# Performance work log

Measured on AMD Instinct MI355X. Metric: run time of the kernel, lower is better.

## Reference

```python
import jax, jax.numpy as jnp
import numpy as np

B, H, W = 4, 64, 64
DIM, HEADS, HEAD = 768, 12, 64
WIN = 14
MLP_DIM = 4 * DIM
EPS = 1e-5


def _ln(x, g, b):
    mu = jnp.mean(x, axis=-1, keepdims=True)
    var = jnp.mean(jnp.square(x - mu), axis=-1, keepdims=True)
    return (x - mu) * jax.lax.rsqrt(var + EPS) * g + b


def _window_partition(x):
    Bb, Hh, Ww, C = x.shape
    pad_h = (WIN - Hh % WIN) % WIN
    pad_w = (WIN - Ww % WIN) % WIN
    x = jnp.pad(x, ((0, 0), (0, pad_h), (0, pad_w), (0, 0)))
    Hp, Wp = Hh + pad_h, Ww + pad_w
    x = x.reshape(Bb, Hp // WIN, WIN, Wp // WIN, WIN, C)
    win = x.transpose(0, 1, 3, 2, 4, 5).reshape(-1, WIN, WIN, C)
    return win, (Hp, Wp)


def _window_unpartition(win, pad_hw, hw):
    Hp, Wp = pad_hw
    Hh, Ww = hw
    Bb = win.shape[0] // (Hp * Wp // WIN // WIN)
    x = win.reshape(Bb, Hp // WIN, Wp // WIN, WIN, WIN, -1)
    x = x.transpose(0, 1, 3, 2, 4, 5).reshape(Bb, Hp, Wp, -1)
    return x[:, :Hh, :Ww, :]


def _attention(xw, qkv_w, qkv_b, proj_w, proj_b, rel_pos_h, rel_pos_w):
    Bw = xw.shape[0]
    N = WIN * WIN
    qkv = xw.reshape(Bw, N, DIM) @ qkv_w + qkv_b            # [Bw, N, 3*DIM]
    qkv = qkv.reshape(Bw, N, 3, HEADS, HEAD)
    qkv = qkv.transpose(2, 0, 3, 1, 4).reshape(3, Bw * HEADS, N, HEAD)
    q, k, v = qkv[0], qkv[1], qkv[2]
    scale = HEAD ** -0.5
    attn = jnp.einsum('bqc,bkc->bqk', q * scale, k)         # [Bw*HEADS, N, N]
    # decomposed relative position bias (q_size == k_size => plain gather)
    idx = jnp.arange(WIN)[:, None] - jnp.arange(WIN)[None, :] + (WIN - 1)
    Rh = rel_pos_h[idx]
    Rw = rel_pos_w[idx]
    r_q = q.reshape(-1, WIN, WIN, HEAD)
    rel_h = jnp.einsum('bhwc,hkc->bhwk', r_q, Rh)
    rel_w = jnp.einsum('bhwc,wkc->bhwk', r_q, Rw)
    attn = attn.reshape(-1, WIN, WIN, WIN, WIN) + rel_h[..., None] + rel_w[..., None, :]
    attn = jax.nn.softmax(attn.reshape(-1, N, N), axis=-1)
    out = attn @ v                                          # [Bw*HEADS, N, HEAD]
    out = out.reshape(Bw, HEADS, WIN, WIN, HEAD).transpose(0, 2, 3, 1, 4)
    out = out.reshape(Bw, WIN, WIN, DIM)
    return out @ proj_w + proj_b


def setup_inputs() -> dict:
    key = jax.random.key(0)
    ks = jax.random.split(key, 8)
    s = 0.02
    return {
        'x': jax.random.normal(ks[0], (B, H, W, DIM), jnp.float32),
        'norm1_g': jnp.ones((DIM,), jnp.float32),
        'norm1_b': jnp.zeros((DIM,), jnp.float32),
        'qkv_w': jax.random.normal(ks[1], (DIM, 3 * DIM), jnp.float32) * s,
        'qkv_b': jnp.zeros((3 * DIM,), jnp.float32),
        'proj_w': jax.random.normal(ks[2], (DIM, DIM), jnp.float32) * s,
        'proj_b': jnp.zeros((DIM,), jnp.float32),
        'rel_pos_h': jax.random.normal(ks[3], (2 * WIN - 1, HEAD), jnp.float32) * s,
        'rel_pos_w': jax.random.normal(ks[4], (2 * WIN - 1, HEAD), jnp.float32) * s,
        'norm2_g': jnp.ones((DIM,), jnp.float32),
        'norm2_b': jnp.zeros((DIM,), jnp.float32),
        'mlp_w1': jax.random.normal(ks[5], (DIM, MLP_DIM), jnp.float32) * s,
        'mlp_b1': jnp.zeros((MLP_DIM,), jnp.float32),
        'mlp_w2': jax.random.normal(ks[6], (MLP_DIM, DIM), jnp.float32) * s,
        'mlp_b2': jnp.zeros((DIM,), jnp.float32),
    }


def reference(x, norm1_g, norm1_b, qkv_w, qkv_b, proj_w, proj_b,
              rel_pos_h, rel_pos_w, norm2_g, norm2_b,
              mlp_w1, mlp_b1, mlp_w2, mlp_b2):
    shortcut = x
    x = _ln(x, norm1_g, norm1_b)
    win, pad_hw = _window_partition(x)
    win = _attention(win, qkv_w, qkv_b, proj_w, proj_b, rel_pos_h, rel_pos_w)
    x = _window_unpartition(win, pad_hw, (H, W))
    x = shortcut + x
    y = _ln(x, norm2_g, norm2_b)
    y = jax.nn.gelu(y @ mlp_w1 + mlp_b1, approximate=False) @ mlp_w2 + mlp_b2
    return x + y
```

## Files before the change

kernel.cpp:

```cpp
#include <hip/hip_runtime.h>
#include <hip/hip_bf16.h>
#include <math.h>

#define DIMC 768
#define NHEADS 12
#define WINSZ 14
#define NTOK 196
#define TOKENS 16384

using bf = __hip_bfloat16;
typedef __attribute__((ext_vector_type(4))) float f32x4;
typedef __attribute__((ext_vector_type(8))) short bf16x8;

typedef __attribute__((address_space(3))) void lds_void_t;
typedef const __attribute__((address_space(1))) void gmem_void_t;

__device__ inline float bfu2f(ushort u) { return __uint_as_float((uint)u << 16); }
__device__ inline ushort f2bu(float f) {
    bf t = __float2bfloat16(f);
    return __builtin_bit_cast(ushort, t);
}

__global__ __launch_bounds__(256) void transpose_k(const float* __restrict__ in,
                                                   ushort* __restrict__ out, int R, int C) {
    long i = (long)blockIdx.x * 256 + threadIdx.x;
    if (i >= (long)R * C) return;
    int r = (int)(i / C), c = (int)(i % C);
    out[(long)c * R + r] = f2bu(in[i]);
}

__device__ inline float blk_sum(float v, float* wred, int tid) {
    for (int m = 32; m; m >>= 1) v += __shfl_xor(v, m);
    if ((tid & 63) == 0) wred[tid >> 6] = v;
    __syncthreads();
    float r = wred[0] + wred[1] + wred[2] + wred[3];
    __syncthreads();
    return r;
}

__global__ __launch_bounds__(256) void ln_k(const float* __restrict__ x, const float* __restrict__ g,
                                            const float* __restrict__ bb, ushort* __restrict__ out) {
    int row = blockIdx.x, tid = threadIdx.x;
    const float* xr = x + (size_t)row * DIMC;
    __shared__ float wred[4];
    float v0 = xr[tid], v1 = xr[tid + 256], v2 = xr[tid + 512];
    float mean = blk_sum(v0 + v1 + v2, wred, tid) * (1.f / 768.f);
    float d0 = v0 - mean, d1 = v1 - mean, d2 = v2 - mean;
    float var = blk_sum(d0 * d0 + d1 * d1 + d2 * d2, wred, tid) * (1.f / 768.f);
    float rs = rsqrtf(var + 1e-5f);
    ushort* o = out + (size_t)row * DIMC;
    o[tid]       = f2bu(d0 * rs * g[tid]       + bb[tid]);
    o[tid + 256] = f2bu(d1 * rs * g[tid + 256] + bb[tid + 256]);
    o[tid + 512] = f2bu(d2 * rs * g[tid + 512] + bb[tid + 512]);
}

enum { EPI_BIAS = 0, EPI_GELU = 1, EPI_PROJRES = 2, EPI_ACC = 3, EPI_RESOUT = 4 };

template <int EPI>
__global__ __launch_bounds__(256) void gemm_k(const ushort* __restrict__ A, int lda,
                                              const ushort* __restrict__ Bt, int ldb,
                                              const float* __restrict__ bias,
                                              ushort* __restrict__ outb,
                                              float* __restrict__ outf,
                                              const float* __restrict__ xorig,
                                              float* __restrict__ x2,
                                              int N, int K) {
    __shared__ ushort lA0[2][128 * 32];
    __shared__ ushort lA1[2][128 * 32];
    __shared__ ushort lB0[2][128 * 32];
    __shared__ ushort lB1[2][128 * 32];

    const int nwg = gridDim.x * gridDim.y;
    const int l = blockIdx.y * gridDim.x + blockIdx.x;
    const int nl = (l & 7) * (nwg >> 3) + (l >> 3);
    const int bx = nl % gridDim.x, by = nl / gridDim.x;
    const int bm = by * 128, bn = bx * 128;

    const int tid = threadIdx.x, wave = tid >> 6, lane = tid & 63;
    const int wy = wave >> 1, wx = wave & 1;
    const int lm = lane & 15, quad = lane >> 4;

    f32x4 acc[4][4];
#pragma unroll
    for (int r = 0; r < 4; ++r)
#pragma unroll
        for (int s = 0; s < 4; ++s) acc[r][s] = (f32x4){0.f, 0.f, 0.f, 0.f};

    const int c0 = wave * 2, c1 = wave * 2 + 1;
    const int srcg = (lane & 3) ^ ((lane >> 3) & 3);
    const ushort* Ab = A + (size_t)(bm + (lane >> 2)) * lda + srcg * 8;
    const ushort* Bb = Bt + (size_t)(bn + (lane >> 2)) * ldb + srcg * 8;
    const size_t a16 = (size_t)16 * lda, b16 = (size_t)16 * ldb;

    auto stage = [&](int bi, int k0) {
        __builtin_amdgcn_global_load_lds((gmem_void_t*)(Ab + (size_t)c0 * a16 + k0),
                                         (lds_void_t*)&lA0[bi][c0 * 512], 16, 0, 0);
        __builtin_amdgcn_global_load_lds((gmem_void_t*)(Ab + (size_t)c0 * a16 + k0 + 32),
                                         (lds_void_t*)&lA1[bi][c0 * 512], 16, 0, 0);
        __builtin_amdgcn_global_load_lds((gmem_void_t*)(Ab + (size_t)c1 * a16 + k0),
                                         (lds_void_t*)&lA0[bi][c1 * 512], 16, 0, 0);
        __builtin_amdgcn_global_load_lds((gmem_void_t*)(Ab + (size_t)c1 * a16 + k0 + 32),
                                         (lds_void_t*)&lA1[bi][c1 * 512], 16, 0, 0);
        __builtin_amdgcn_global_load_lds((gmem_void_t*)(Bb + (size_t)c0 * b16 + k0),
                                         (lds_void_t*)&lB0[bi][c0 * 512], 16, 0, 0);
        __builtin_amdgcn_global_load_lds((gmem_void_t*)(Bb + (size_t)c0 * b16 + k0 + 32),
                                         (lds_void_t*)&lB1[bi][c0 * 512], 16, 0, 0);
        __builtin_amdgcn_global_load_lds((gmem_void_t*)(Bb + (size_t)c1 * b16 + k0),
                                         (lds_void_t*)&lB0[bi][c1 * 512], 16, 0, 0);
        __builtin_amdgcn_global_load_lds((gmem_void_t*)(Bb + (size_t)c1 * b16 + k0 + 32),
                                         (lds_void_t*)&lB1[bi][c1 * 512], 16, 0, 0);
    };

    const int rg = (quad ^ ((lm >> 1) & 3)) * 8;
    const int nt = K >> 6;

    stage(0, 0);
    __syncthreads();

    for (int t = 0; t < nt; ++t) {
        const int cur = t & 1;
        if (t + 1 < nt) stage(cur ^ 1, (t + 1) * 64);

        bf16x8 af0[4], af1[4], bv0[4], bv1[4];
#pragma unroll
        for (int r = 0; r < 4; ++r) {
            af0[r] = *(const bf16x8*)&lA0[cur][(wy * 64 + r * 16 + lm) * 32 + rg];
            af1[r] = *(const bf16x8*)&lA1[cur][(wy * 64 + r * 16 + lm) * 32 + rg];
        }
#pragma unroll
        for (int s = 0; s < 4; ++s) {
            bv0[s] = *(const bf16x8*)&lB0[cur][(wx * 64 + s * 16 + lm) * 32 + rg];
            bv1[s] = *(const bf16x8*)&lB1[cur][(wx * 64 + s * 16 + lm) * 32 + rg];
        }
#pragma unroll
        for (int r = 0; r < 4; ++r)
#pragma unroll
            for (int s = 0; s < 4; ++s) {
                acc[r][s] = __builtin_amdgcn_mfma_f32_16x16x32_bf16(af0[r], bv0[s], acc[r][s], 0, 0, 0);
                acc[r][s] = __builtin_amdgcn_mfma_f32_16x16x32_bf16(af1[r], bv1[s], acc[r][s], 0, 0, 0);
            }
        __syncthreads();
    }

#pragma unroll
    for (int s = 0; s < 4; ++s) {
        int col = bn + wx * 64 + s * 16 + lm;
        float bvl = (EPI == EPI_ACC) ? 0.f : bias[col];
#pragma unroll
        for (int r = 0; r < 4; ++r) {
#pragma unroll
            for (int i = 0; i < 4; ++i) {
                int row = bm + wy * 64 + r * 16 + quad * 4 + i;
                float v = acc[r][s][i] + bvl;
                size_t idx = (size_t)row * N + col;
                if constexpr (EPI == EPI_BIAS) {
                    outb[idx] = f2bu(v);
                } else if constexpr (EPI == EPI_GELU) {
                    outb[idx] = f2bu(0.5f * v * (1.f + erff(v * 0.70710678118f)));
                } else if constexpr (EPI == EPI_PROJRES) {
                    x2[idx] = xorig[idx] + v;
                } else if constexpr (EPI == EPI_ACC) {
                    x2[idx] += v;
                } else {
                    outf[idx] = x2[idx] + v;
                }
            }
        }
    }
}

__global__ __launch_bounds__(256) void attn_k(const ushort* __restrict__ qkv,
                                              const float* __restrict__ qkvb,
                                              const float* __restrict__ relh,
                                              const float* __restrict__ relw,
                                              ushort* __restrict__ aout) {
    const int win = blockIdx.x / NHEADS, head = blockIdx.x % NHEADS;
    const int b = win / 25, wi = win % 25, wr = wi / 5, wc = wi % 5;
    const int hmax = (wr == 4) ? 8 : WINSZ, wmax = (wc == 4) ? 8 : WINSZ;
    const int hoff = head * 64;
    const int tid = threadIdx.x, wave = tid >> 6, lane = tid & 63;
    const int c = lane & 15, quad = lane >> 4;

    __shared__ ushort Ksw[224 * 64];
    __shared__ ushort vTs[64 * 264];
    __shared__ ushort wscr[4][640];

    for (int t = tid; t < 224 * 8; t += 256) {
        int n = t >> 3, ck = t & 7;
        int kh = n >> 4, kw = n & 15;
        uint4 vals;
        if (kw < WINSZ && kh < hmax && kw < wmax) {
            size_t tok = ((size_t)(b * 64 + wr * WINSZ + kh) * 64 + wc * WINSZ + kw);
            vals = *(const uint4*)(qkv + tok * 2304 + 768 + hoff + ck * 8);
        } else if (kw < WINSZ) {
            union { uint4 u; ushort s[8]; } tmp;
#pragma unroll
            for (int j = 0; j < 8; ++j) tmp.s[j] = f2bu(qkvb[768 + hoff + ck * 8 + j]);
            vals = tmp.u;
        } else {
            vals = (uint4){0u, 0u, 0u, 0u};
        }
        *(uint4*)&Ksw[n * 64 + ((ck ^ (n & 7)) * 8)] = vals;
    }
    for (int t = tid; t < 224 * 8; t += 256) {
        int n = t >> 3, dg = t & 7;
        int kh = n >> 4, kw = n & 15;
        union { uint4 u; ushort s[8]; } vals;
        if (kw < WINSZ && kh < hmax && kw < wmax) {
            size_t tok = ((size_t)(b * 64 + wr * WINSZ + kh) * 64 + wc * WINSZ + kw);
            vals.u = *(const uint4*)(qkv + tok * 2304 + 1536 + hoff + dg * 8);
        } else if (kw < WINSZ) {
#pragma unroll
            for (int j = 0; j < 8; ++j) vals.s[j] = f2bu(qkvb[1536 + hoff + dg * 8 + j]);
        } else {
            vals.u = (uint4){0u, 0u, 0u, 0u};
        }
        int kchunk = n >> 3;
#pragma unroll
        for (int j = 0; j < 8; ++j) {
            int d = dg * 8 + j;
            vTs[d * 264 + ((kchunk ^ dg) * 8) + (n & 7)] = vals.s[j];
        }
    }
    __syncthreads();

    bf16x8 rhB[2][2], rwB[2][2];
#pragma unroll
    for (int nt = 0; nt < 2; ++nt) {
        int j = nt * 16 + c; if (j > 26) j = 26;
#pragma unroll
        for (int ks = 0; ks < 2; ++ks) {
            const float* ph = relh + (size_t)j * 64 + ks * 32 + quad * 8;
            const float* pw = relw + (size_t)j * 64 + ks * 32 + quad * 8;
            bf16x8 h, w;
#pragma unroll
            for (int e = 0; e < 8; ++e) {
                h[e] = (short)f2bu(ph[e]);
                w[e] = (short)f2bu(pw[e]);
            }
            rhB[nt][ks] = h; rwB[nt][ks] = w;
        }
    }

    ushort* scr = &wscr[wave][0];
    const int lane48 = lane & 48;

    for (int qh = wave; qh < hmax; qh += 4) {
        int qw = c < wmax ? c : (wmax - 1);
        size_t qtok = ((size_t)(b * 64 + wr * WINSZ + qh) * 64 + wc * WINSZ + qw);
        bf16x8 aq0 = *(const bf16x8*)(qkv + qtok * 2304 + hoff + quad * 8);
        bf16x8 aq1 = *(const bf16x8*)(qkv + qtok * 2304 + hoff + 32 + quad * 8);

        f32x4 z = (f32x4){0.f, 0.f, 0.f, 0.f};
        f32x4 dh0 = __builtin_amdgcn_mfma_f32_16x16x32_bf16(aq0, rhB[0][0], z, 0, 0, 0);
        dh0 = __builtin_amdgcn_mfma_f32_16x16x32_bf16(aq1, rhB[0][1], dh0, 0, 0, 0);
        f32x4 dh1 = __builtin_amdgcn_mfma_f32_16x16x32_bf16(aq0, rhB[1][0], z, 0, 0, 0);
        dh1 = __builtin_amdgcn_mfma_f32_16x16x32_bf16(aq1, rhB[1][1], dh1, 0, 0, 0);
        f32x4 dw0 = __builtin_amdgcn_mfma_f32_16x16x32_bf16(aq0, rwB[0][0], z, 0, 0, 0);
        dw0 = __builtin_amdgcn_mfma_f32_16x16x32_bf16(aq1, rwB[0][1], dw0, 0, 0, 0);
        f32x4 dw1 = __builtin_amdgcn_mfma_f32_16x16x32_bf16(aq0, rwB[1][0], z, 0, 0, 0);
        dw1 = __builtin_amdgcn_mfma_f32_16x16x32_bf16(aq1, rwB[1][1], dw1, 0, 0, 0);

#pragma unroll
        for (int i = 0; i < 4; ++i) {
            scr[(quad * 4 + i) * 28 + c] = f2bu(dh0[i]);
            if (c < 12) scr[(quad * 4 + i) * 28 + 16 + c] = f2bu(dh1[i]);
        }

        float bw[4];
#pragma unroll
        for (int i = 0; i < 4; ++i) {
            int m = quad * 4 + i;
            int j = m - c + 13; int jc = j < 0 ? 0 : j;
            int addr = (lane48 | (jc & 15)) << 2;
            int t0 = __builtin_amdgcn_ds_bpermute(addr, __float_as_int(dw0[i]));
            int t1 = __builtin_amdgcn_ds_bpermute(addr, __float_as_int(dw1[i]));
            bw[i] = (jc >= 16) ? __int_as_float(t1) : __int_as_float(t0);
        }

        f32x4 s[14];
#pragma unroll
        for (int kh = 0; kh < 14; ++kh) {
            int n = kh * 16 + c;
            int n7 = n & 7;
            bf16x8 kb0 = *(const bf16x8*)&Ksw[n * 64 + ((0 * 4 + quad) ^ n7) * 8];
            bf16x8 kb1 = *(const bf16x8*)&Ksw[n * 64 + ((1 * 4 + quad) ^ n7) * 8];
            f32x4 acc = __builtin_amdgcn_mfma_f32_16x16x32_bf16(aq0, kb0, z, 0, 0, 0);
            acc = __builtin_amdgcn_mfma_f32_16x16x32_bf16(aq1, kb1, acc, 0, 0, 0);
            int jstar = qh + 13 - kh;
#pragma unroll
            for (int i = 0; i < 4; ++i) {
                float dh = bfu2f(scr[(quad * 4 + i) * 28 + jstar]);
                float v = fmaf(0.125f, acc[i], dh + bw[i]);
                acc[i] = (c < WINSZ) ? v : -1e30f;
            }
            s[kh] = acc;
        }

        float inv[4];
#pragma unroll
        for (int i = 0; i < 4; ++i) {
            float mx = s[0][i];
#pragma unroll
            for (int kh = 1; kh < 14; ++kh) mx = fmaxf(mx, s[kh][i]);
            mx = fmaxf(mx, __shfl_xor(mx, 1));
            mx = fmaxf(mx, __shfl_xor(mx, 2));
            mx = fmaxf(mx, __shfl_xor(mx, 4));
            mx = fmaxf(mx, __shfl_xor(mx, 8));
            float sum = 0.f;
#pragma unroll
            for (int kh = 0; kh < 14; ++kh) {
                float e = __expf(s[kh][i] - mx);
                s[kh][i] = e;
                sum += e;
            }
            sum += __shfl_xor(sum, 1);
            sum += __shfl_xor(sum, 2);
            sum += __shfl_xor(sum, 4);
            sum += __shfl_xor(sum, 8);
            inv[i] = 1.f / sum;
        }

        f32x4 o[4] = {z, z, z, z};
#pragma unroll
        for (int cc = 0; cc < 7; ++cc) {
#pragma unroll
            for (int i = 0; i < 4; ++i) {
                scr[(quad * 4 + i) * 40 + c]      = f2bu(s[2 * cc][i] * inv[i]);
                scr[(quad * 4 + i) * 40 + 16 + c] = f2bu(s[2 * cc + 1][i] * inv[i]);
            }
            bf16x8 ap = *(const bf16x8*)&scr[c * 40 + quad * 8];
#pragma unroll
            for (int vt = 0; vt < 4; ++vt) {
                int d = vt * 16 + c;
                int dgr = (d >> 3) & 7;
                bf16x8 vb = *(const bf16x8*)&vTs[d * 264 + (((cc * 4 + quad) ^ dgr) * 8)];
                o[vt] = __builtin_amdgcn_mfma_f32_16x16x32_bf16(ap, vb, o[vt], 0, 0, 0);
            }
        }

#pragma unroll
        for (int i = 0; i < 4; ++i) {
            int qwp = quad * 4 + i;
            if (qwp < wmax) {
                size_t otok = ((size_t)(b * 64 + wr * WINSZ + qh) * 64 + wc * WINSZ + qwp);
#pragma unroll
                for (int vt = 0; vt < 4; ++vt)
                    aout[otok * 768 + hoff + vt * 16 + c] = f2bu(o[vt][i]);
            }
        }
    }
}

extern "C" void kernel_launch(void* const* d_in, const int* in_sizes, int n_in,
                              void* d_out, int out_size, void* d_ws, size_t ws_size,
                              hipStream_t stream) {
    const float* x      = (const float*)d_in[0];
    const float* n1g    = (const float*)d_in[1];
    const float* n1b    = (const float*)d_in[2];
    const float* qkv_w  = (const float*)d_in[3];
    const float* qkv_b  = (const float*)d_in[4];
    const float* proj_w = (const float*)d_in[5];
    const float* proj_b = (const float*)d_in[6];
    const float* relh   = (const float*)d_in[7];
    const float* relw   = (const float*)d_in[8];
    const float* n2g    = (const float*)d_in[9];
    const float* n2b    = (const float*)d_in[10];
    const float* w1     = (const float*)d_in[11];
    const float* b1     = (const float*)d_in[12];
    const float* w2     = (const float*)d_in[13];
    const float* b2     = (const float*)d_in[14];
    float* out = (float*)d_out;

    char* ws = (char*)d_ws;
    size_t off = 0;
    auto alloc = [&](size_t bytes) -> void* {
        void* p = ws + off;
        off += (bytes + 255) & ~(size_t)255;
        return p;
    };

    ushort* lnbuf  = (ushort*)alloc((size_t)TOKENS * DIMC * 2);
    ushort* qkvbuf = (ushort*)alloc((size_t)TOKENS * 2304 * 2);
    float* x2      = (float*)alloc((size_t)TOKENS * DIMC * 4);
    ushort* qkvT   = (ushort*)alloc((size_t)2304 * 768 * 2);
    ushort* projT  = (ushort*)alloc((size_t)768 * 768 * 2);
    ushort* w1T    = (ushort*)alloc((size_t)3072 * 768 * 2);
    ushort* w2T    = (ushort*)alloc((size_t)768 * 3072 * 2);
    ushort* aout   = lnbuf;
    ushort* hc     = qkvbuf;

    transpose_k<<<(768 * 2304 + 255) / 256, 256, 0, stream>>>(qkv_w, qkvT, 768, 2304);
    transpose_k<<<(768 * 768 + 255) / 256, 256, 0, stream>>>(proj_w, projT, 768, 768);
    transpose_k<<<(768 * 3072 + 255) / 256, 256, 0, stream>>>(w1, w1T, 768, 3072);
    transpose_k<<<(3072 * 768 + 255) / 256, 256, 0, stream>>>(w2, w2T, 3072, 768);

    ln_k<<<TOKENS, 256, 0, stream>>>(x, n1g, n1b, lnbuf);

    dim3 gq(2304 / 128, TOKENS / 128);
    gemm_k<EPI_BIAS><<<gq, 256, 0, stream>>>(lnbuf, DIMC, qkvT, DIMC, qkv_b, qkvbuf,
                                             nullptr, nullptr, nullptr, 2304, DIMC);

    attn_k<<<100 * NHEADS, 256, 0, stream>>>(qkvbuf, qkv_b, relh, relw, aout);

    dim3 gp(DIMC / 128, TOKENS / 128);
    gemm_k<EPI_PROJRES><<<gp, 256, 0, stream>>>(aout, DIMC, projT, DIMC, proj_b, nullptr,
                                                nullptr, x, x2, DIMC, DIMC);

    ln_k<<<TOKENS, 256, 0, stream>>>(x2, n2g, n2b, lnbuf);

    dim3 gh(1536 / 128, TOKENS / 128);
    for (int c = 0; c < 2; ++c) {
        gemm_k<EPI_GELU><<<gh, 256, 0, stream>>>(lnbuf, DIMC, w1T + (size_t)c * 1536 * 768, DIMC,
                                                 b1 + c * 1536, hc, nullptr, nullptr, nullptr,
                                                 1536, DIMC);
        if (c == 0)
            gemm_k<EPI_ACC><<<gp, 256, 0, stream>>>(hc, 1536, w2T + (size_t)c * 1536, 3072,
                                                    b2, nullptr, nullptr, nullptr, x2, DIMC, 1536);
        else
            gemm_k<EPI_RESOUT><<<gp, 256, 0, stream>>>(hc, 1536, w2T + (size_t)c * 1536, 3072,
                                                       b2, nullptr, out, nullptr, x2, DIMC, 1536);
    }
}
```

Measured before the change: 678.7 us.

## Read K fragments directly from global memory instead of staging in LDS

Removes the shared-memory K tile and its cooperative fill loop. Each wave now loads its K MFMA operands straight from the qkv buffer per key row, substituting the broadcast key bias for padded positions. Occupancy is also hinted with launch_bounds(256,4), since LDS use drops by about 28KB. The trade is repeated global/L2 reads of K by every wave and per-query-row iteration instead of one shared staging pass, which adds latency inside the inner MFMA loop.

```diff
diff --git a/kernel.cpp b/kernel.cpp
--- a/kernel.cpp
+++ b/kernel.cpp
@@ -169,11 +169,11 @@
     }
 }
 
-__global__ __launch_bounds__(256) void attn_k(const ushort* __restrict__ qkv,
-                                              const float* __restrict__ qkvb,
-                                              const float* __restrict__ relh,
-                                              const float* __restrict__ relw,
-                                              ushort* __restrict__ aout) {
+__global__ __launch_bounds__(256, 4) void attn_k(const ushort* __restrict__ qkv,
+                                                 const float* __restrict__ qkvb,
+                                                 const float* __restrict__ relh,
+                                                 const float* __restrict__ relw,
+                                                 ushort* __restrict__ aout) {
     const int win = blockIdx.x / NHEADS, head = blockIdx.x % NHEADS;
     const int b = win / 25, wi = win % 25, wr = wi / 5, wc = wi % 5;
     const int hmax = (wr == 4) ? 8 : WINSZ, wmax = (wc == 4) ? 8 : WINSZ;
@@ -181,27 +181,9 @@
     const int tid = threadIdx.x, wave = tid >> 6, lane = tid & 63;
     const int c = lane & 15, quad = lane >> 4;
 
-    __shared__ ushort Ksw[224 * 64];
     __shared__ ushort vTs[64 * 264];
     __shared__ ushort wscr[4][640];
 
-    for (int t = tid; t < 224 * 8; t += 256) {
-        int n = t >> 3, ck = t & 7;
-        int kh = n >> 4, kw = n & 15;
-        uint4 vals;
-        if (kw < WINSZ && kh < hmax && kw < wmax) {
-            size_t tok = ((size_t)(b * 64 + wr * WINSZ + kh) * 64 + wc * WINSZ + kw);
-            vals = *(const uint4*)(qkv + tok * 2304 + 768 + hoff + ck * 8);
-        } else if (kw < WINSZ) {
-            union { uint4 u; ushort s[8]; } tmp;
-#pragma unroll
-            for (int j = 0; j < 8; ++j) tmp.s[j] = f2bu(qkvb[768 + hoff + ck * 8 + j]);
-            vals = tmp.u;
-        } else {
-            vals = (uint4){0u, 0u, 0u, 0u};
-        }
-        *(uint4*)&Ksw[n * 64 + ((ck ^ (n & 7)) * 8)] = vals;
-    }
     for (int t = tid; t < 224 * 8; t += 256) {
         int n = t >> 3, dg = t & 7;
         int kh = n >> 4, kw = n & 15;
@@ -241,6 +223,18 @@
             rhB[nt][ks] = h; rwB[nt][ks] = w;
         }
     }
+
+    bf16x8 kbias0, kbias1;
+#pragma unroll
+    for (int j = 0; j < 8; ++j) {
+        kbias0[j] = (short)f2bu(qkvb[768 + hoff + quad * 8 + j]);
+        kbias1[j] = (short)f2bu(qkvb[768 + hoff + 32 + quad * 8 + j]);
+    }
+    const int ccl = (c < wmax) ? c : (wmax - 1);
+    const bool cval = (c < wmax);
+    const ushort* Kp = qkv + ((size_t)(b * 64 + wr * WINSZ) * 64 + wc * WINSZ + ccl) * 2304
+                     + 768 + hoff + quad * 8;
+    const size_t krow = (size_t)64 * 2304;
 
     ushort* scr = &wscr[wave][0];
     const int lane48 = lane & 48;
@@ -281,10 +275,16 @@
         f32x4 s[14];
 #pragma unroll
         for (int kh = 0; kh < 14; ++kh) {
-            int n = kh * 16 + c;
-            int n7 = n & 7;
-            bf16x8 kb0 = *(const bf16x8*)&Ksw[n * 64 + ((0 * 4 + quad) ^ n7) * 8];
-            bf16x8 kb1 = *(const bf16x8*)&Ksw[n * 64 + ((1 * 4 + quad) ^ n7) * 8];
+            bf16x8 kb0, kb1;
+            if (kh < 8 || kh < hmax) {
+                const ushort* p = Kp + (size_t)kh * krow;
+                bf16x8 g0 = *(const bf16x8*)p;
+                bf16x8 g1 = *(const bf16x8*)(p + 32);
+                kb0 = cval ? g0 : kbias0;
+                kb1 = cval ? g1 : kbias1;
+            } else {
+                kb0 = kbias0; kb1 = kbias1;
+            }
             f32x4 acc = __builtin_amdgcn_mfma_f32_16x16x32_bf16(aq0, kb0, z, 0, 0, 0);
             acc = __builtin_amdgcn_mfma_f32_16x16x32_bf16(aq1, kb1, acc, 0, 0, 0);
             int jstar = qh + 13 - kh;
```

Result: slower. 885.7 us (+30.5%).

## Process two query rows per wave in attention to reuse K/V LDS fragments

Applied to the files above, without the earlier changes.

The attention kernel now has each wave handle two query rows at once (qh and qh+4), sharing each loaded K and V fragment across two MFMA chains. Per-wave scratch is doubled to hold bias and probability tiles for both rows. This is meant to halve K/V LDS reads per query row and add independent MFMA work for latency hiding. The cost is much higher register pressure from two 14-tile score arrays, and redundant compute when the second row is a clamped dummy. A launch-bounds minimum of 2 blocks per CU is also added, which may force spills.

```diff
diff --git a/kernel.cpp b/kernel.cpp
--- a/kernel.cpp
+++ b/kernel.cpp
@@ -169,11 +169,11 @@
     }
 }
 
-__global__ __launch_bounds__(256) void attn_k(const ushort* __restrict__ qkv,
-                                              const float* __restrict__ qkvb,
-                                              const float* __restrict__ relh,
-                                              const float* __restrict__ relw,
-                                              ushort* __restrict__ aout) {
+__global__ __launch_bounds__(256, 2) void attn_k(const ushort* __restrict__ qkv,
+                                                 const float* __restrict__ qkvb,
+                                                 const float* __restrict__ relh,
+                                                 const float* __restrict__ relw,
+                                                 ushort* __restrict__ aout) {
     const int win = blockIdx.x / NHEADS, head = blockIdx.x % NHEADS;
     const int b = win / 25, wi = win % 25, wr = wi / 5, wc = wi % 5;
     const int hmax = (wr == 4) ? 8 : WINSZ, wmax = (wc == 4) ? 8 : WINSZ;
@@ -183,7 +183,7 @@
 
     __shared__ ushort Ksw[224 * 64];
     __shared__ ushort vTs[64 * 264];
-    __shared__ ushort wscr[4][640];
+    __shared__ ushort wscr[4][2][640];
 
     for (int t = tid; t < 224 * 8; t += 256) {
         int n = t >> 3, ck = t & 7;
@@ -242,111 +242,152 @@
         }
     }
 
-    ushort* scr = &wscr[wave][0];
     const int lane48 = lane & 48;
-
-    for (int qh = wave; qh < hmax; qh += 4) {
-        int qw = c < wmax ? c : (wmax - 1);
-        size_t qtok = ((size_t)(b * 64 + wr * WINSZ + qh) * 64 + wc * WINSZ + qw);
-        bf16x8 aq0 = *(const bf16x8*)(qkv + qtok * 2304 + hoff + quad * 8);
-        bf16x8 aq1 = *(const bf16x8*)(qkv + qtok * 2304 + hoff + 32 + quad * 8);
-
-        f32x4 z = (f32x4){0.f, 0.f, 0.f, 0.f};
-        f32x4 dh0 = __builtin_amdgcn_mfma_f32_16x16x32_bf16(aq0, rhB[0][0], z, 0, 0, 0);
-        dh0 = __builtin_amdgcn_mfma_f32_16x16x32_bf16(aq1, rhB[0][1], dh0, 0, 0, 0);
-        f32x4 dh1 = __builtin_amdgcn_mfma_f32_16x16x32_bf16(aq0, rhB[1][0], z, 0, 0, 0);
-        dh1 = __builtin_amdgcn_mfma_f32_16x16x32_bf16(aq1, rhB[1][1], dh1, 0, 0, 0);
-        f32x4 dw0 = __builtin_amdgcn_mfma_f32_16x16x32_bf16(aq0, rwB[0][0], z, 0, 0, 0);
-        dw0 = __builtin_amdgcn_mfma_f32_16x16x32_bf16(aq1, rwB[0][1], dw0, 0, 0, 0);
-        f32x4 dw1 = __builtin_amdgcn_mfma_f32_16x16x32_bf16(aq0, rwB[1][0], z, 0, 0, 0);
-        dw1 = __builtin_amdgcn_mfma_f32_16x16x32_bf16(aq1, rwB[1][1], dw1, 0, 0, 0);
-
-#pragma unroll
-        for (int i = 0; i < 4; ++i) {
-            scr[(quad * 4 + i) * 28 + c] = f2bu(dh0[i]);
-            if (c < 12) scr[(quad * 4 + i) * 28 + 16 + c] = f2bu(dh1[i]);
-        }
-
-        float bw[4];
-#pragma unroll
-        for (int i = 0; i < 4; ++i) {
-            int m = quad * 4 + i;
-            int j = m - c + 13; int jc = j < 0 ? 0 : j;
-            int addr = (lane48 | (jc & 15)) << 2;
-            int t0 = __builtin_amdgcn_ds_bpermute(addr, __float_as_int(dw0[i]));
-            int t1 = __builtin_amdgcn_ds_bpermute(addr, __float_as_int(dw1[i]));
-            bw[i] = (jc >= 16) ? __int_as_float(t1) : __int_as_float(t0);
-        }
-
-        f32x4 s[14];
+    const int qw = c < wmax ? c : (wmax - 1);
+    f32x4 z = (f32x4){0.f, 0.f, 0.f, 0.f};
+
+    for (int qp = 0; qp < 2; ++qp) {
+        const int qh0 = wave + qp * 8;
+        if (qh0 >= hmax) break;
+        const int qh1r = qh0 + 4;
+        const bool v1 = qh1r < hmax;
+        const int qhc[2] = {qh0, v1 ? qh1r : hmax - 1};
+
+        bf16x8 aqA[2], aqB[2];
+#pragma unroll
+        for (int ch = 0; ch < 2; ++ch) {
+            size_t qtok = ((size_t)(b * 64 + wr * WINSZ + qhc[ch]) * 64 + wc * WINSZ + qw);
+            aqA[ch] = *(const bf16x8*)(qkv + qtok * 2304 + hoff + quad * 8);
+            aqB[ch] = *(const bf16x8*)(qkv + qtok * 2304 + hoff + 32 + quad * 8);
+        }
+
+        f32x4 dh0[2], dh1[2], dw0[2], dw1[2];
+#pragma unroll
+        for (int ch = 0; ch < 2; ++ch) {
+            dh0[ch] = __builtin_amdgcn_mfma_f32_16x16x32_bf16(aqA[ch], rhB[0][0], z, 0, 0, 0);
+            dh0[ch] = __builtin_amdgcn_mfma_f32_16x16x32_bf16(aqB[ch], rhB[0][1], dh0[ch], 0, 0, 0);
+            dh1[ch] = __builtin_amdgcn_mfma_f32_16x16x32_bf16(aqA[ch], rhB[1][0], z, 0, 0, 0);
+            dh1[ch] = __builtin_amdgcn_mfma_f32_16x16x32_bf16(aqB[ch], rhB[1][1], dh1[ch], 0, 0, 0);
+            dw0[ch] = __builtin_amdgcn_mfma_f32_16x16x32_bf16(aqA[ch], rwB[0][0], z, 0, 0, 0);
+            dw0[ch] = __builtin_amdgcn_mfma_f32_16x16x32_bf16(aqB[ch], rwB[0][1], dw0[ch], 0, 0, 0);
+            dw1[ch] = __builtin_amdgcn_mfma_f32_16x16x32_bf16(aqA[ch], rwB[1][0], z, 0, 0, 0);
+            dw1[ch] = __builtin_amdgcn_mfma_f32_16x16x32_bf16(aqB[ch], rwB[1][1], dw1[ch], 0, 0, 0);
+        }
+
+#pragma unroll
+        for (int ch = 0; ch < 2; ++ch) {
+            ushort* scp = &wscr[wave][ch][0];
+#pragma unroll
+            for (int i = 0; i < 4; ++i) {
+                scp[(quad * 4 + i) * 28 + c] = f2bu(dh0[ch][i]);
+                if (c < 12) scp[(quad * 4 + i) * 28 + 16 + c] = f2bu(dh1[ch][i]);
+            }
+        }
+
+        float bw[2][4];
+#pragma unroll
+        for (int ch = 0; ch < 2; ++ch)
+#pragma unroll
+            for (int i = 0; i < 4; ++i) {
+                int m = quad * 4 + i;
+                int j = m - c + 13; int jc = j < 0 ? 0 : j;
+                int addr = (lane48 | (jc & 15)) << 2;
+                int t0 = __builtin_amdgcn_ds_bpermute(addr, __float_as_int(dw0[ch][i]));
+                int t1 = __builtin_amdgcn_ds_bpermute(addr, __float_as_int(dw1[ch][i]));
+                bw[ch][i] = (jc >= 16) ? __int_as_float(t1) : __int_as_float(t0);
+            }
+
+        f32x4 s[2][14];
 #pragma unroll
         for (int kh = 0; kh < 14; ++kh) {
             int n = kh * 16 + c;
             int n7 = n & 7;
             bf16x8 kb0 = *(const bf16x8*)&Ksw[n * 64 + ((0 * 4 + quad) ^ n7) * 8];
             bf16x8 kb1 = *(const bf16x8*)&Ksw[n * 64 + ((1 * 4 + quad) ^ n7) * 8];
-            f32x4 acc = __builtin_amdgcn_mfma_f32_16x16x32_bf16(aq0, kb0, z, 0, 0, 0);
-            acc = __builtin_amdgcn_mfma_f32_16x16x32_bf16(aq1, kb1, acc, 0, 0, 0);
-            int jstar = qh + 13 - kh;
+#pragma unroll
+            for (int ch = 0; ch < 2; ++ch) {
+                f32x4 acc = __builtin_amdgcn_mfma_f32_16x16x32_bf16(aqA[ch], kb0, z, 0, 0, 0);
+                acc = __builtin_amdgcn_mfma_f32_16x16x32_bf16(aqB[ch], kb1, acc, 0, 0, 0);
+                int jstar = qhc[ch] + 13 - kh;
+                const ushort* scp = &wscr[wave][ch][0];
+#pragma unroll
+                for (int i = 0; i < 4; ++i) {
+                    float dh = bfu2f(scp[(quad * 4 + i) * 28 + jstar]);
+                    float v = fmaf(0.125f, acc[i], dh + bw[ch][i]);
+                    acc[i] = (c < WINSZ) ? v : -1e30f;
+                }
+                s[ch][kh] = acc;
+            }
+        }
+
+        float inv[2][4];
+#pragma unroll
+        for (int ch = 0; ch < 2; ++ch)
 #pragma unroll
             for (int i = 0; i < 4; ++i) {
-                float dh = bfu2f(scr[(quad * 4 + i) * 28 + jstar]);
-                float v = fmaf(0.125f, acc[i], dh + bw[i]);
-                acc[i] = (c < WINSZ) ? v : -1e30f;
-            }
-            s[kh] = acc;
-        }
-
-        float inv[4];
-#pragma unroll
-        for (int i = 0; i < 4; ++i) {
-            float mx = s[0][i];
-#pragma unroll
-            for (int kh = 1; kh < 14; ++kh) mx = fmaxf(mx, s[kh][i]);
-            mx = fmaxf(mx, __shfl_xor(mx, 1));
-            mx = fmaxf(mx, __shfl_xor(mx, 2));
-            mx = fmaxf(mx, __shfl_xor(mx, 4));
-            mx = fmaxf(mx, __shfl_xor(mx, 8));
-            float sum = 0.f;
-#pragma unroll
-            for (int kh = 0; kh < 14; ++kh) {
-                float e = __expf(s[kh][i] - mx);
-                s[kh][i] = e;
-                sum += e;
-            }
-            sum += __shfl_xor(sum, 1);
-            sum += __shfl_xor(sum, 2);
-            sum += __shfl_xor(sum, 4);
-            sum += __shfl_xor(sum, 8);
-            inv[i] = 1.f / sum;
-        }
-
-        f32x4 o[4] = {z, z, z, z};
+                float mx = s[ch][0][i];
+#pragma unroll
+                for (int kh = 1; kh < 14; ++kh) mx = fmaxf(mx, s[ch][kh][i]);
+                mx = fmaxf(mx, __shfl_xor(mx, 1));
+                mx = fmaxf(mx, __shfl_xor(mx, 2));
+                mx = fmaxf(mx, __shfl_xor(mx, 4));
+                mx = fmaxf(mx, __shfl_xor(mx, 8));
+                float sum = 0.f;
+#pragma unroll
+                for (int kh = 0; kh < 14; ++kh) {
+                    float e = __expf(s[ch][kh][i] - mx);
+                    s[ch][kh][i] = e;
+                    sum += e;
+                }
+                sum += __shfl_xor(sum, 1);
+                sum += __shfl_xor(sum, 2);
+                sum += __shfl_xor(sum, 4);
+                sum += __shfl_xor(sum, 8);
+                inv[ch][i] = 1.f / sum;
+            }
+
+        f32x4 o[2][4];
+#pragma unroll
+        for (int ch = 0; ch < 2; ++ch)
+#pragma unroll
+            for (int vt = 0; vt < 4; ++vt) o[ch][vt] = z;
+
 #pragma unroll
         for (int cc = 0; cc < 7; ++cc) {
-#pragma unroll
-            for (int i = 0; i < 4; ++i) {
-                scr[(quad * 4 + i) * 40 + c]      = f2bu(s[2 * cc][i] * inv[i]);
-                scr[(quad * 4 + i) * 40 + 16 + c] = f2bu(s[2 * cc + 1][i] * inv[i]);
-            }
-            bf16x8 ap = *(const bf16x8*)&scr[c * 40 + quad * 8];
+            bf16x8 ap[2];
+#pragma unroll
+            for (int ch = 0; ch < 2; ++ch) {
+                ushort* scp = &wscr[wave][ch][0];
+#pragma unroll
+                for (int i = 0; i < 4; ++i) {
+                    scp[(quad * 4 + i) * 40 + c]      = f2bu(s[ch][2 * cc][i] * inv[ch][i]);
+                    scp[(quad * 4 + i) * 40 + 16 + c] = f2bu(s[ch][2 * cc + 1][i] * inv[ch][i]);
+                }
+                ap[ch] = *(const bf16x8*)&scp[c * 40 + quad * 8];
+            }
 #pragma unroll
             for (int vt = 0; vt < 4; ++vt) {
                 int d = vt * 16 + c;
                 int dgr = (d >> 3) & 7;
                 bf16x8 vb = *(const bf16x8*)&vTs[d * 264 + (((cc * 4 + quad) ^ dgr) * 8)];
-                o[vt] = __builtin_amdgcn_mfma_f32_16x16x32_bf16(ap, vb, o[vt], 0, 0, 0);
-            }
-        }
-
-#pragma unroll
-        for (int i = 0; i < 4; ++i) {
-            int qwp = quad * 4 + i;
-            if (qwp < wmax) {
-                size_t otok = ((size_t)(b * 64 + wr * WINSZ + qh) * 64 + wc * WINSZ + qwp);
-#pragma unroll
-                for (int vt = 0; vt < 4; ++vt)
-                    aout[otok * 768 + hoff + vt * 16 + c] = f2bu(o[vt][i]);
+#pragma unroll
+                for (int ch = 0; ch < 2; ++ch)
+                    o[ch][vt] = __builtin_amdgcn_mfma_f32_16x16x32_bf16(ap[ch], vb, o[ch][vt], 0, 0, 0);
+            }
+        }
+
+#pragma unroll
+        for (int ch = 0; ch < 2; ++ch) {
+            if (ch == 1 && !v1) break;
+#pragma unroll
+            for (int i = 0; i < 4; ++i) {
+                int qwp = quad * 4 + i;
+                if (qwp < wmax) {
+                    size_t otok = ((size_t)(b * 64 + wr * WINSZ + qhc[ch]) * 64 + wc * WINSZ + qwp);
+#pragma unroll
+                    for (int vt = 0; vt < 4; ++vt)
+                        aout[otok * 768 + hoff + vt * 16 + c] = f2bu(o[ch][vt][i]);
+                }
             }
         }
     }
```

New measurement: 709.3 us. 4.5% more time.

## Deepen GEMM LDS pipeline to four K=32 stages and tile weight transposes

Applied to the files above, without the earlier changes.

The GEMM main loop moves from double-buffered K=64 tiles to a four-slot ring of K=32 tiles with three loads in flight. It uses explicit vmcnt waits and a single barrier per step, and issues the next load after reading fragments, so global loads overlap MFMA work more deeply. Separately, the weight transpose kernel now uses a 32x32 shared-memory tile so both reads and writes are coalesced. The finer K step doubles the number of barriers and the hand-counted vmcnt values must match the per-stage load count exactly.

```diff
diff --git a/kernel.cpp b/kernel.cpp
--- a/kernel.cpp
+++ b/kernel.cpp
@@ -23,10 +23,21 @@
 
 __global__ __launch_bounds__(256) void transpose_k(const float* __restrict__ in,
                                                    ushort* __restrict__ out, int R, int C) {
-    long i = (long)blockIdx.x * 256 + threadIdx.x;
-    if (i >= (long)R * C) return;
-    int r = (int)(i / C), c = (int)(i % C);
-    out[(long)c * R + r] = f2bu(in[i]);
+    __shared__ ushort tile[32][33];
+    const int nbx = C >> 5;
+    const int bx = blockIdx.x % nbx, by = blockIdx.x / nbx;
+    const int tx = threadIdx.x & 31, ty = threadIdx.x >> 5;
+#pragma unroll
+    for (int p = 0; p < 4; ++p) {
+        int r = by * 32 + ty + p * 8;
+        tile[ty + p * 8][tx] = f2bu(in[(size_t)r * C + bx * 32 + tx]);
+    }
+    __syncthreads();
+#pragma unroll
+    for (int p = 0; p < 4; ++p) {
+        int c = bx * 32 + ty + p * 8;
+        out[(size_t)c * R + by * 32 + tx] = tile[tx][ty + p * 8];
+    }
 }
 
 __device__ inline float blk_sum(float v, float* wred, int tid) {
@@ -65,10 +76,8 @@
                                               const float* __restrict__ xorig,
                                               float* __restrict__ x2,
                                               int N, int K) {
-    __shared__ ushort lA0[2][128 * 32];
-    __shared__ ushort lA1[2][128 * 32];
-    __shared__ ushort lB0[2][128 * 32];
-    __shared__ ushort lB1[2][128 * 32];
+    __shared__ ushort hA[4][128 * 32];
+    __shared__ ushort hB[4][128 * 32];
 
     const int nwg = gridDim.x * gridDim.y;
     const int l = blockIdx.y * gridDim.x + blockIdx.x;
@@ -92,54 +101,47 @@
     const ushort* Bb = Bt + (size_t)(bn + (lane >> 2)) * ldb + srcg * 8;
     const size_t a16 = (size_t)16 * lda, b16 = (size_t)16 * ldb;
 
-    auto stage = [&](int bi, int k0) {
+    auto stageH = [&](int bi, int k0) {
         __builtin_amdgcn_global_load_lds((gmem_void_t*)(Ab + (size_t)c0 * a16 + k0),
-                                         (lds_void_t*)&lA0[bi][c0 * 512], 16, 0, 0);
-        __builtin_amdgcn_global_load_lds((gmem_void_t*)(Ab + (size_t)c0 * a16 + k0 + 32),
-                                         (lds_void_t*)&lA1[bi][c0 * 512], 16, 0, 0);
+                                         (lds_void_t*)&hA[bi][c0 * 512], 16, 0, 0);
         __builtin_amdgcn_global_load_lds((gmem_void_t*)(Ab + (size_t)c1 * a16 + k0),
-                                         (lds_void_t*)&lA0[bi][c1 * 512], 16, 0, 0);
-        __builtin_amdgcn_global_load_lds((gmem_void_t*)(Ab + (size_t)c1 * a16 + k0 + 32),
-                                         (lds_void_t*)&lA1[bi][c1 * 512], 16, 0, 0);
+                                         (lds_void_t*)&hA[bi][c1 * 512], 16, 0, 0);
         __builtin_amdgcn_global_load_lds((gmem_void_t*)(Bb + (size_t)c0 * b16 + k0),
-                                         (lds_void_t*)&lB0[bi][c0 * 512], 16, 0, 0);
-        __builtin_amdgcn_global_load_lds((gmem_void_t*)(Bb + (size_t)c0 * b16 + k0 + 32),
-                                         (lds_void_t*)&lB1[bi][c0 * 512], 16, 0, 0);
+                                         (lds_void_t*)&hB[bi][c0 * 512], 16, 0, 0);
         __builtin_amdgcn_global_load_lds((gmem_void_t*)(Bb + (size_t)c1 * b16 + k0),
-                                         (lds_void_t*)&lB0[bi][c1 * 512], 16, 0, 0);
-        __builtin_amdgcn_global_load_lds((gmem_void_t*)(Bb + (size_t)c1 * b16 + k0 + 32),
-                                         (lds_void_t*)&lB1[bi][c1 * 512], 16, 0, 0);
+                                         (lds_void_t*)&hB[bi][c1 * 512], 16, 0, 0);
     };
 
     const int rg = (quad ^ ((lm >> 1) & 3)) * 8;
-    const int nt = K >> 6;
-
-    stage(0, 0);
-    __syncthreads();
-
-    for (int t = 0; t < nt; ++t) {
-        const int cur = t & 1;
-        if (t + 1 < nt) stage(cur ^ 1, (t + 1) * 64);
-
-        bf16x8 af0[4], af1[4], bv0[4], bv1[4];
-#pragma unroll
-        for (int r = 0; r < 4; ++r) {
-            af0[r] = *(const bf16x8*)&lA0[cur][(wy * 64 + r * 16 + lm) * 32 + rg];
-            af1[r] = *(const bf16x8*)&lA1[cur][(wy * 64 + r * 16 + lm) * 32 + rg];
-        }
-#pragma unroll
-        for (int s = 0; s < 4; ++s) {
-            bv0[s] = *(const bf16x8*)&lB0[cur][(wx * 64 + s * 16 + lm) * 32 + rg];
-            bv1[s] = *(const bf16x8*)&lB1[cur][(wx * 64 + s * 16 + lm) * 32 + rg];
-        }
+    const int H = K >> 5;
+
+    stageH(0, 0);
+    if (H > 1) stageH(1, 32);
+    if (H > 2) stageH(2, 64);
+
+    for (int h = 0; h < H; ++h) {
+        if (h + 2 < H)      asm volatile("s_waitcnt vmcnt(8)" ::: "memory");
+        else if (h + 1 < H) asm volatile("s_waitcnt vmcnt(4)" ::: "memory");
+        else                asm volatile("s_waitcnt vmcnt(0)" ::: "memory");
+        __builtin_amdgcn_s_barrier();
+        __builtin_amdgcn_sched_barrier(0);
+
+        const int bi = h & 3;
+        bf16x8 af[4], bv[4];
 #pragma unroll
         for (int r = 0; r < 4; ++r)
-#pragma unroll
-            for (int s = 0; s < 4; ++s) {
-                acc[r][s] = __builtin_amdgcn_mfma_f32_16x16x32_bf16(af0[r], bv0[s], acc[r][s], 0, 0, 0);
-                acc[r][s] = __builtin_amdgcn_mfma_f32_16x16x32_bf16(af1[r], bv1[s], acc[r][s], 0, 0, 0);
-            }
-        __syncthreads();
+            af[r] = *(const bf16x8*)&hA[bi][(wy * 64 + r * 16 + lm) * 32 + rg];
+#pragma unroll
+        for (int s = 0; s < 4; ++s)
+            bv[s] = *(const bf16x8*)&hB[bi][(wx * 64 + s * 16 + lm) * 32 + rg];
+
+        if (h + 3 < H) stageH((h + 3) & 3, (h + 3) * 32);
+
+#pragma unroll
+        for (int r = 0; r < 4; ++r)
+#pragma unroll
+            for (int s = 0; s < 4; ++s)
+                acc[r][s] = __builtin_amdgcn_mfma_f32_16x16x32_bf16(af[r], bv[s], acc[r][s], 0, 0, 0);
     }
 
 #pragma unroll
@@ -390,10 +392,10 @@
     ushort* aout   = lnbuf;
     ushort* hc     = qkvbuf;
 
-    transpose_k<<<(768 * 2304 + 255) / 256, 256, 0, stream>>>(qkv_w, qkvT, 768, 2304);
-    transpose_k<<<(768 * 768 + 255) / 256, 256, 0, stream>>>(proj_w, projT, 768, 768);
-    transpose_k<<<(768 * 3072 + 255) / 256, 256, 0, stream>>>(w1, w1T, 768, 3072);
-    transpose_k<<<(3072 * 768 + 255) / 256, 256, 0, stream>>>(w2, w2T, 3072, 768);
+    transpose_k<<<(768 / 32) * (2304 / 32), 256, 0, stream>>>(qkv_w, qkvT, 768, 2304);
+    transpose_k<<<(768 / 32) * (768 / 32), 256, 0, stream>>>(proj_w, projT, 768, 768);
+    transpose_k<<<(768 / 32) * (3072 / 32), 256, 0, stream>>>(w1, w1T, 768, 3072);
+    transpose_k<<<(3072 / 32) * (768 / 32), 256, 0, stream>>>(w2, w2T, 3072, 768);
 
     ln_k<<<TOKENS, 256, 0, stream>>>(x, n1g, n1b, lnbuf);
 
```

Result: faster. 660.9 us (-2.6%).
